# Kernel tuning notes

Measured on AMD Instinct MI355X. Metric: run time of the kernel, lower is better.

Reference implementation:

```python
import jax, jax.numpy as jnp
import numpy as np

B, S, H = 8, 2048, 1024
NEG = 1.0e10


def setup_inputs() -> dict:
    key = jax.random.key(0)
    ks = jax.random.split(key, 9)
    scale = 1.0 / np.sqrt(H)
    x = jax.random.normal(ks[0], (B, S, H), dtype=jnp.float32)
    Wq = jax.random.normal(ks[1], (H, H), dtype=jnp.float32) * scale
    bq = jnp.zeros((H,), dtype=jnp.float32)
    Wk = jax.random.normal(ks[2], (H, H), dtype=jnp.float32) * scale
    bk = jnp.zeros((H,), dtype=jnp.float32)
    Wv = jax.random.normal(ks[3], (H, H), dtype=jnp.float32) * scale
    bv = jnp.zeros((H,), dtype=jnp.float32)
    gamma = jnp.ones((H,), dtype=jnp.float32)
    beta = jnp.zeros((H,), dtype=jnp.float32)
    return {"x": x, "Wq": Wq, "bq": bq, "Wk": Wk, "bk": bk,
            "Wv": Wv, "bv": bv, "gamma": gamma, "beta": beta}


def _layernorm(y, gamma, beta, eps=1e-5):
    mu = jnp.mean(y, axis=-1, keepdims=True)
    var = jnp.var(y, axis=-1, keepdims=True)
    return (y - mu) * jax.lax.rsqrt(var + eps) * gamma + beta


def reference(x, Wq, bq, Wk, bk, Wv, bv, gamma, beta):
    # QKV projections (single head, no 1/sqrt(d) scaling, per original code)
    q = x @ Wq + bq                       # [B, S, H]
    k = x @ Wk + bk                       # [B, S, H]
    v = x @ Wv + bv                       # [B, S, H]
    scores = jnp.einsum('bsh,bth->bst', q, k)   # [B, S, S]
    # non-standard multiplicative-subtractive causal mask
    mask = jnp.tril(jnp.ones((S, S), dtype=scores.dtype))  # [S, S]
    scores = scores * mask - NEG * (1.0 - mask)
    probs = jax.nn.softmax(scores, axis=-1)
    attn = jnp.einsum('bst,bth->bsh', probs, v)
    return _layernorm(v + attn, gamma, beta)
```

## Files before the change

### kernel.cpp

```cpp
#include <hip/hip_runtime.h>

#define SQ 2048
#define HD 1024
#define NB 8
#define NTOT (NB*SQ)
#define NT2 8
#define NTRI2 36
#define CE ((long long)NTRI2*65536)

typedef _Float16 f16x8 __attribute__((ext_vector_type(8)));
typedef float f32x4 __attribute__((ext_vector_type(4)));
typedef short s16x8 __attribute__((ext_vector_type(8)));
typedef unsigned short u16;

__device__ __forceinline__ u16 f2h(float x){
  _Float16 h = (_Float16)x;
  u16 u; __builtin_memcpy(&u, &h, 2); return u;
}

#define STG(gp, lp) __builtin_amdgcn_global_load_lds( \
    (const __attribute__((address_space(1))) unsigned*)(gp), \
    (__attribute__((address_space(3))) unsigned*)(lp), 16, 0, 0)

template<int EPI>
__global__ __launch_bounds__(512, 2)
void gemm8(const u16* __restrict__ A, const u16* __restrict__ B,
           float* Cf, u16* Ch, u16* Vt,
           const float* __restrict__ b0, const float* __restrict__ b1,
           const float* __restrict__ b2,
           int K, int lda, int ldb, int ldc,
           long long sA, long long sB, long long sC)
{
  const int z = blockIdx.z;
  int bi, bj, tri = 0;
  if (EPI == 1){
    int t = blockIdx.x;
    int i = (int)((sqrtf(8.f * (float)t + 1.f) - 1.f) * 0.5f);
    while ((i + 1) * (i + 2) / 2 <= t) ++i;
    while (i * (i + 1) / 2 > t) --i;
    bi = i;  bj = t - i * (i + 1) / 2;  tri = t;
  } else {
    bi = blockIdx.x;  bj = blockIdx.y;
    if (EPI == 2) tri = bi * (bi + 1) / 2;
  }

  __shared__ short lds[65536];

  const int tid  = threadIdx.x;
  const int lane = tid & 63, w = tid >> 6;
  const int wm2 = w >> 2, wn4 = w & 3;
  const int lrow = lane & 15, kgrp = lane >> 4;

  const long long rowA = (long long)bi * 256;
  const long long colB = (long long)bj * 256;

  const int rt = tid >> 3;
  const int gs = (tid & 7) ^ (rt & 7);

  const u16 *sAp[4], *sBp[4];
  if (EPI == 2){
    const u16* Pb = A + (long long)z * sA + (long long)tri * 65536;
    #pragma unroll
    for (int i = 0; i < 4; i++)
      sAp[i] = Pb + (i * 64 + rt) * 256 + gs * 8;
  } else {
    const u16* Ab = A + (EPI == 0 ? 0LL : (long long)z * sA);
    #pragma unroll
    for (int i = 0; i < 4; i++)
      sAp[i] = Ab + (rowA + i * 64 + rt) * (long long)lda + gs * 8;
  }
  {
    const u16* Bb = B + (long long)z * sB;
    #pragma unroll
    for (int i = 0; i < 4; i++)
      sBp[i] = Bb + (colB + i * 64 + rt) * (long long)ldb + gs * 8;
  }

  #define ADST(buf,i) (lds + (buf) * 32768 +         (i) * 4096 + w * 512)
  #define BDST(buf,i) (lds + (buf) * 32768 + 16384 + (i) * 4096 + w * 512)

  const int fl = lrow & 7;
  const int swzk[2] = { ((0 + kgrp) ^ fl) * 8, ((4 + kgrp) ^ fl) * 8 };
  const int arow = (wm2 * 128 + lrow) * 64;
  const int brow = 16384 + (wn4 * 64 + lrow) * 64;

  f32x4 acc[8][4];
  const f32x4 zf = {0.f, 0.f, 0.f, 0.f};
  #pragma unroll
  for (int m = 0; m < 8; m++)
    #pragma unroll
    for (int n = 0; n < 4; n++) acc[m][n] = zf;

  int KT = K >> 6;
  if (EPI == 2){ int t = (bi + 1) * 4; if (t < KT) KT = t; }

  auto advance = [&](int tS){
    long long advA = 64;
    if (EPI == 2) advA = ((tS & 3) == 3) ? (65536 - 192) : 64;
    #pragma unroll
    for (int i = 0; i < 4; i++){ sAp[i] += advA; sBp[i] += 64; }
  };

  #pragma unroll
  for (int i = 0; i < 4; i++) STG(sAp[i], ADST(0, i));
  #pragma unroll
  for (int i = 0; i < 4; i++) STG(sBp[i], BDST(0, i));
  advance(0);
  __syncthreads();

  int cur = 0;
  for (int kt = 0; kt < KT; ++kt){
    const bool pf = (kt + 1 < KT);
    const short* Ab = lds + cur * 32768;
    const int nb = cur ^ 1;

    #pragma unroll
    for (int qm = 0; qm < 2; qm++){
      f16x8 aq[4][2];
      #pragma unroll
      for (int m4 = 0; m4 < 4; m4++)
        #pragma unroll
        for (int ks = 0; ks < 2; ks++)
          aq[m4][ks] = *(const f16x8*)(Ab + arow + (qm * 4 + m4) * 1024 + swzk[ks]);

      #pragma unroll
      for (int qn = 0; qn < 2; qn++){
        if (pf && qm == 0 && qn == 0){
          #pragma unroll
          for (int i = 0; i < 4; i++) STG(sAp[i], ADST(nb, i));
        }
        if (pf && qm == 0 && qn == 1){
          #pragma unroll
          for (int i = 0; i < 4; i++) STG(sBp[i], BDST(nb, i));
        }
        f16x8 bq[2][2];
        #pragma unroll
        for (int n2 = 0; n2 < 2; n2++)
          #pragma unroll
          for (int ks = 0; ks < 2; ks++)
            bq[n2][ks] = *(const f16x8*)(Ab + brow + (qn * 2 + n2) * 1024 + swzk[ks]);

        __builtin_amdgcn_s_setprio(1);
        #pragma unroll
        for (int n2 = 0; n2 < 2; n2++)
          #pragma unroll
          for (int m4 = 0; m4 < 4; m4++)
            #pragma unroll
            for (int ks = 0; ks < 2; ks++)
              acc[qm * 4 + m4][qn * 2 + n2] =
                __builtin_amdgcn_mfma_f32_16x16x32_f16(aq[m4][ks], bq[n2][ks],
                                                       acc[qm * 4 + m4][qn * 2 + n2], 0, 0, 0);
        __builtin_amdgcn_s_setprio(0);
        __builtin_amdgcn_s_barrier();
      }
    }
    if (pf) advance(kt + 1);
    __syncthreads();
    cur ^= 1;
  }
  #undef ADST
  #undef BDST

  if (EPI == 0){
    if (z < 2){
      u16* c = Ch + (long long)z * sC;
      const float* bias = z ? b1 : b0;
      #pragma unroll
      for (int n = 0; n < 4; n++){
        int col = (int)colB + wn4 * 64 + n * 16 + lrow;
        float ba = bias[col];
        #pragma unroll
        for (int m = 0; m < 8; m++){
          long long r = rowA + wm2 * 128 + m * 16 + kgrp * 4;
          #pragma unroll
          for (int j = 0; j < 4; j++)
            c[(r + j) * ldc + col] = f2h(acc[m][n][j] + ba);
        }
      }
    } else {
      #pragma unroll
      for (int n = 0; n < 4; n++){
        int col = (int)colB + wn4 * 64 + n * 16 + lrow;
        float ba = b2[col];
        #pragma unroll
        for (int m = 0; m < 8; m++){
          long long r = rowA + wm2 * 128 + m * 16 + kgrp * 4;
          int bb = (int)(r >> 11);
          int s  = (int)(r & 2047);
          u16* vtc = Vt + ((long long)bb * HD + col) * SQ + s;
          #pragma unroll
          for (int j = 0; j < 4; j++){
            float v = acc[m][n][j] + ba;
            Cf[(r + j) * ldc + col] = v;
            vtc[j] = f2h(v);
          }
        }
      }
    }
  } else if (EPI == 1){
    float* cf = Cf + (long long)z * sC + (long long)tri * 65536;
    #pragma unroll
    for (int n = 0; n < 4; n++){
      int col = wn4 * 64 + n * 16 + lrow;
      #pragma unroll
      for (int m = 0; m < 8; m++){
        int r = wm2 * 128 + m * 16 + kgrp * 4;
        #pragma unroll
        for (int j = 0; j < 4; j++)
          cf[(r + j) * 256 + col] = acc[m][n][j];
      }
    }
  } else {
    float* cf = Cf + (long long)z * sC;
    #pragma unroll
    for (int n = 0; n < 4; n++){
      int col = (int)colB + wn4 * 64 + n * 16 + lrow;
      #pragma unroll
      for (int m = 0; m < 8; m++){
        long long r = rowA + wm2 * 128 + m * 16 + kgrp * 4;
        #pragma unroll
        for (int j = 0; j < 4; j++){
          long long o = (r + j) * ldc + col;
          cf[o] = acc[m][n][j] + cf[o];
        }
      }
    }
  }
}

__global__ __launch_bounds__(256)
void prep_x(const float* __restrict__ X, u16* __restrict__ Xh)
{
  const long long n8 = (long long)NTOT * HD / 8;
  for (long long i = (long long)blockIdx.x * 256 + threadIdx.x; i < n8;
       i += (long long)gridDim.x * 256){
    const float* p = X + i * 8;
    float4 a = *(const float4*)p;
    float4 b = *(const float4*)(p + 4);
    float f[8] = {a.x, a.y, a.z, a.w, b.x, b.y, b.z, b.w};
    s16x8 h;
    #pragma unroll
    for (int j = 0; j < 8; j++) h[j] = (short)f2h(f[j]);
    *(s16x8*)&Xh[i * 8] = h;
  }
}

__global__ void prep_w(const float* __restrict__ Wq, const float* __restrict__ Wk,
                       const float* __restrict__ Wv, u16* __restrict__ Wt)
{
  __shared__ float t[32][33];
  const float* Win = (blockIdx.z == 0) ? Wq : (blockIdx.z == 1) ? Wk : Wv;
  const size_t zo = (size_t)blockIdx.z * HD * HD;
  int n0 = blockIdx.x * 32, k0 = blockIdx.y * 32;
  int tx = threadIdx.x, ty = threadIdx.y;
  #pragma unroll
  for (int i = 0; i < 4; i++)
    t[ty + 8*i][tx] = Win[(size_t)(k0 + ty + 8*i) * HD + n0 + tx];
  __syncthreads();
  #pragma unroll
  for (int i = 0; i < 4; i++)
    Wt[zo + (size_t)(n0 + ty + 8*i) * HD + k0 + tx] = f2h(t[tx][ty + 8*i]);
}

__global__ __launch_bounds__(256)
void softmax_causal(const float* __restrict__ SC, u16* __restrict__ P)
{
  const int s = blockIdx.x;
  const int i = s >> 8;
  const int tri = i * (i + 1) / 2;
  const long long base = (long long)blockIdx.y * CE + (long long)tri * 65536
                       + (long long)(s & 255) * 256;
  const float* scb = SC + base;
  u16* pb = P + base;

  __shared__ float buf[SQ];
  __shared__ float red[4];
  const int tid = threadIdx.x, lane = tid & 63, wid = tid >> 6;

  float m = -3.4e38f;
  for (int t = tid; t <= s; t += 256){
    float v = scb[(t >> 8) * 65536 + (t & 255)];
    buf[t] = v; m = fmaxf(m, v);
  }
  #pragma unroll
  for (int o = 32; o; o >>= 1) m = fmaxf(m, __shfl_xor(m, o));
  if (lane == 0) red[wid] = m;
  __syncthreads();
  m = fmaxf(fmaxf(red[0], red[1]), fmaxf(red[2], red[3]));
  __syncthreads();

  float sum = 0.f;
  for (int t = tid; t <= s; t += 256){ float e = __expf(buf[t] - m); buf[t] = e; sum += e; }
  #pragma unroll
  for (int o = 32; o; o >>= 1) sum += __shfl_xor(sum, o);
  if (lane == 0) red[wid] = sum;
  __syncthreads();
  sum = red[0] + red[1] + red[2] + red[3];
  const float inv = 1.f / sum;

  const int lim = (i + 1) << 8;
  for (int t = tid; t < lim; t += 256)
    pb[(t >> 8) * 65536 + (t & 255)] = (t <= s) ? f2h(buf[t] * inv) : (u16)0;
}

__global__ __launch_bounds__(256)
void layernorm_inplace(float* __restrict__ Y, const float* __restrict__ gamma,
                       const float* __restrict__ beta)
{
  float* y = Y + (long long)blockIdx.x * HD;
  const int tid = threadIdx.x, lane = tid & 63, wid = tid >> 6;
  float xv[4];
  float s = 0.f, ss = 0.f;
  #pragma unroll
  for (int i = 0; i < 4; i++){
    float v = y[tid + i * 256];
    xv[i] = v; s += v; ss += v * v;
  }
  #pragma unroll
  for (int o = 32; o; o >>= 1){ s += __shfl_xor(s, o); ss += __shfl_xor(ss, o); }
  __shared__ float r1[4], r2[4];
  if (lane == 0){ r1[wid] = s; r2[wid] = ss; }
  __syncthreads();
  s  = r1[0] + r1[1] + r1[2] + r1[3];
  ss = r2[0] + r2[1] + r2[2] + r2[3];
  const float mu   = s * (1.f / HD);
  const float var  = ss * (1.f / HD) - mu * mu;
  const float rstd = rsqrtf(var + 1e-5f);
  #pragma unroll
  for (int i = 0; i < 4; i++){
    int c = tid + i * 256;
    y[c] = (xv[i] - mu) * rstd * gamma[c] + beta[c];
  }
}

extern "C" void kernel_launch(void* const* d_in, const int* in_sizes, int n_in,
                              void* d_out, int out_size, void* d_ws, size_t ws_size,
                              hipStream_t stream)
{
  const float* x     = (const float*)d_in[0];
  const float* Wq    = (const float*)d_in[1];
  const float* bq    = (const float*)d_in[2];
  const float* Wk    = (const float*)d_in[3];
  const float* bk    = (const float*)d_in[4];
  const float* Wv    = (const float*)d_in[5];
  const float* bv    = (const float*)d_in[6];
  const float* gamma = (const float*)d_in[7];
  const float* beta  = (const float*)d_in[8];
  float* out = (float*)d_out;

  char* wsp = (char*)d_ws;
  size_t off = 0;
  auto alloc = [&](size_t bytes) -> char* {
    char* p = wsp + off;
    off = (off + bytes + 255) & ~(size_t)255;
    return p;
  };

  u16* Wt = (u16*)alloc(3ULL * HD * HD * 2);
  u16* QK = (u16*)alloc(2ULL * NTOT * HD * 2);
  u16* Vt = (u16*)alloc((size_t)NB * HD * SQ * 2);

  size_t rem = (ws_size > off) ? (ws_size - off) : 0;
  size_t perb = (size_t)CE * 6;
  int G = (int)(rem / perb);
  if (G > NB) G = NB;
  if (G < 1)  G = 1;
  u16*   xh = (u16*)(wsp + off);
  float* SC = (float*)(wsp + off);
  u16*   P  = (u16*)(wsp + off + (size_t)G * CE * 4);

  u16* Qh = QK;
  u16* Kh = QK + (size_t)NTOT * HD;
  float* V = out;

  prep_x<<<dim3(2048), dim3(256), 0, stream>>>(x, xh);
  prep_w<<<dim3(HD/32, HD/32, 3), dim3(32, 8), 0, stream>>>(Wq, Wk, Wv, Wt);

  gemm8<0><<<dim3(NTOT/256, HD/256, 3), 512, 0, stream>>>(
      xh, Wt, V, QK, Vt, bq, bk, bv,
      HD, HD, HD, HD,
      0LL, (long long)HD * HD, (long long)NTOT * HD);

  for (int g0 = 0; g0 < NB; g0 += G){
    int g = (G < NB - g0) ? G : (NB - g0);
    gemm8<1><<<dim3(NTRI2, 1, g), 512, 0, stream>>>(
        Qh + (size_t)g0 * SQ * HD, Kh + (size_t)g0 * SQ * HD,
        SC, nullptr, nullptr, nullptr, nullptr, nullptr,
        HD, HD, HD, 256,
        (long long)SQ * HD, (long long)SQ * HD, CE);
    softmax_causal<<<dim3(SQ, g), 256, 0, stream>>>(SC, P);
    gemm8<2><<<dim3(NT2, HD/256, g), 512, 0, stream>>>(
        P, Vt + (size_t)g0 * HD * SQ,
        out + (size_t)g0 * SQ * HD, nullptr, nullptr, nullptr, nullptr, nullptr,
        SQ, 256, SQ, HD,
        CE, (long long)HD * SQ, (long long)SQ * HD);
  }

  layernorm_inplace<<<dim3(NTOT), 256, 0, stream>>>(out, gamma, beta);
}
```

Measured before the change: 379.6 us.

## Switch GEMM mainloop to 4-stage K=32 pipeline with vmcnt-based waits

Replaces the double-buffered K=64 LDS pipeline with a four-stage ring of K=32 tiles, prefetching three stages ahead and waiting with explicit s_waitcnt vmcnt counts instead of full __syncthreads. The LDS layout and swizzle are reorganised so each wave reads its A/B fragments for a single K=32 step. The aim is to hide global-load latency better and cut barrier stalls, at the cost of more loop iterations, more barriers per unit of K, and reliance on exact vmcnt accounting for correctness.

```diff
diff --git a/kernel.cpp b/kernel.cpp
--- a/kernel.cpp
+++ b/kernel.cpp
@@ -44,7 +44,7 @@
     if (EPI == 2) tri = bi * (bi + 1) / 2;
   }
 
-  __shared__ short lds[65536];
+  __shared__ short lds[4 * 16384];
 
   const int tid  = threadIdx.x;
   const int lane = tid & 63, w = tid >> 6;
@@ -55,34 +55,32 @@
   const long long colB = (long long)bj * 256;
 
   const int rt = tid >> 3;
-  const int gs = (tid & 7) ^ (rt & 7);
-
-  const u16 *sAp[4], *sBp[4];
+  const int qp = (tid & 7) ^ (rt & 7);
+  const int kq = qp & 3;
+  const int rh = (qp >> 2) << 7;
+
+  const u16 *sAp[2], *sBp[2];
   if (EPI == 2){
     const u16* Pb = A + (long long)z * sA + (long long)tri * 65536;
     #pragma unroll
-    for (int i = 0; i < 4; i++)
-      sAp[i] = Pb + (i * 64 + rt) * 256 + gs * 8;
+    for (int i = 0; i < 2; i++)
+      sAp[i] = Pb + (i * 64 + rt + rh) * 256 + kq * 8;
   } else {
     const u16* Ab = A + (EPI == 0 ? 0LL : (long long)z * sA);
     #pragma unroll
-    for (int i = 0; i < 4; i++)
-      sAp[i] = Ab + (rowA + i * 64 + rt) * (long long)lda + gs * 8;
+    for (int i = 0; i < 2; i++)
+      sAp[i] = Ab + (rowA + i * 64 + rt + rh) * (long long)lda + kq * 8;
   }
   {
     const u16* Bb = B + (long long)z * sB;
     #pragma unroll
-    for (int i = 0; i < 4; i++)
-      sBp[i] = Bb + (colB + i * 64 + rt) * (long long)ldb + gs * 8;
-  }
-
-  #define ADST(buf,i) (lds + (buf) * 32768 +         (i) * 4096 + w * 512)
-  #define BDST(buf,i) (lds + (buf) * 32768 + 16384 + (i) * 4096 + w * 512)
-
-  const int fl = lrow & 7;
-  const int swzk[2] = { ((0 + kgrp) ^ fl) * 8, ((4 + kgrp) ^ fl) * 8 };
-  const int arow = (wm2 * 128 + lrow) * 64;
-  const int brow = 16384 + (wn4 * 64 + lrow) * 64;
+    for (int i = 0; i < 2; i++)
+      sBp[i] = Bb + (colB + i * 64 + rt + rh) * (long long)ldb + kq * 8;
+  }
+
+  const int aoff = lrow * 64 + ((((wm2 << 2) | kgrp) ^ (lrow & 7)) << 3);
+  const int boff = 8192 + ((wn4 & 1) * 64 + lrow) * 64
+                 + (((((wn4 >> 1) << 2) | kgrp) ^ (lrow & 7)) << 3);
 
   f32x4 acc[8][4];
   const f32x4 zf = {0.f, 0.f, 0.f, 0.f};
@@ -91,75 +89,68 @@
     #pragma unroll
     for (int n = 0; n < 4; n++) acc[m][n] = zf;
 
-  int KT = K >> 6;
-  if (EPI == 2){ int t = (bi + 1) * 4; if (t < KT) KT = t; }
-
+  int KT = K >> 5;
+  if (EPI == 2){ int t = (bi + 1) * 8; if (t < KT) KT = t; }
+
+  auto stage = [&](int b){
+    #pragma unroll
+    for (int i = 0; i < 2; i++) STG(sAp[i], lds + b * 16384 +        (i * 8 + w) * 512);
+    #pragma unroll
+    for (int i = 0; i < 2; i++) STG(sBp[i], lds + b * 16384 + 8192 + (i * 8 + w) * 512);
+  };
   auto advance = [&](int tS){
-    long long advA = 64;
-    if (EPI == 2) advA = ((tS & 3) == 3) ? (65536 - 192) : 64;
-    #pragma unroll
-    for (int i = 0; i < 4; i++){ sAp[i] += advA; sBp[i] += 64; }
+    long long advA = 32;
+    if (EPI == 2) advA = ((tS & 7) == 7) ? (65536 - 224) : 32;
+    sAp[0] += advA; sAp[1] += advA; sBp[0] += 32; sBp[1] += 32;
   };
 
-  #pragma unroll
-  for (int i = 0; i < 4; i++) STG(sAp[i], ADST(0, i));
-  #pragma unroll
-  for (int i = 0; i < 4; i++) STG(sBp[i], BDST(0, i));
-  advance(0);
-  __syncthreads();
-
-  int cur = 0;
+  stage(0); advance(0);
+  if (KT > 1){ stage(1); advance(1); }
+  if (KT > 2){ stage(2); advance(2); }
+  if (KT > 2)      { asm volatile("s_waitcnt vmcnt(8)" ::: "memory"); }
+  else if (KT > 1) { asm volatile("s_waitcnt vmcnt(4)" ::: "memory"); }
+  else             { asm volatile("s_waitcnt vmcnt(0)" ::: "memory"); }
+  __builtin_amdgcn_s_barrier();
+
   for (int kt = 0; kt < KT; ++kt){
-    const bool pf = (kt + 1 < KT);
-    const short* Ab = lds + cur * 32768;
-    const int nb = cur ^ 1;
-
-    #pragma unroll
-    for (int qm = 0; qm < 2; qm++){
-      f16x8 aq[4][2];
-      #pragma unroll
-      for (int m4 = 0; m4 < 4; m4++)
-        #pragma unroll
-        for (int ks = 0; ks < 2; ks++)
-          aq[m4][ks] = *(const f16x8*)(Ab + arow + (qm * 4 + m4) * 1024 + swzk[ks]);
-
-      #pragma unroll
-      for (int qn = 0; qn < 2; qn++){
-        if (pf && qm == 0 && qn == 0){
-          #pragma unroll
-          for (int i = 0; i < 4; i++) STG(sAp[i], ADST(nb, i));
-        }
-        if (pf && qm == 0 && qn == 1){
-          #pragma unroll
-          for (int i = 0; i < 4; i++) STG(sBp[i], BDST(nb, i));
-        }
-        f16x8 bq[2][2];
-        #pragma unroll
-        for (int n2 = 0; n2 < 2; n2++)
-          #pragma unroll
-          for (int ks = 0; ks < 2; ks++)
-            bq[n2][ks] = *(const f16x8*)(Ab + brow + (qn * 2 + n2) * 1024 + swzk[ks]);
-
-        __builtin_amdgcn_s_setprio(1);
-        #pragma unroll
-        for (int n2 = 0; n2 < 2; n2++)
-          #pragma unroll
-          for (int m4 = 0; m4 < 4; m4++)
-            #pragma unroll
-            for (int ks = 0; ks < 2; ks++)
-              acc[qm * 4 + m4][qn * 2 + n2] =
-                __builtin_amdgcn_mfma_f32_16x16x32_f16(aq[m4][ks], bq[n2][ks],
-                                                       acc[qm * 4 + m4][qn * 2 + n2], 0, 0, 0);
-        __builtin_amdgcn_s_setprio(0);
-        __builtin_amdgcn_s_barrier();
-      }
-    }
-    if (pf) advance(kt + 1);
-    __syncthreads();
-    cur ^= 1;
-  }
-  #undef ADST
-  #undef BDST
+    const short* Ab = lds + (kt & 3) * 16384;
+    if (kt + 3 < KT){ stage((kt + 3) & 3); advance(kt + 3); }
+
+    f16x8 bfr[4], af[4];
+    #pragma unroll
+    for (int n = 0; n < 4; n++)
+      bfr[n] = *(const f16x8*)(Ab + boff + n * 1024);
+    #pragma unroll
+    for (int m = 0; m < 4; m++)
+      af[m] = *(const f16x8*)(Ab + aoff + m * 1024);
+
+    __builtin_amdgcn_s_setprio(1);
+    #pragma unroll
+    for (int n = 0; n < 4; n++)
+      #pragma unroll
+      for (int m = 0; m < 4; m++)
+        acc[m][n] = __builtin_amdgcn_mfma_f32_16x16x32_f16(af[m], bfr[n], acc[m][n], 0, 0, 0);
+    __builtin_amdgcn_s_setprio(0);
+    __builtin_amdgcn_s_barrier();
+
+    #pragma unroll
+    for (int m = 0; m < 4; m++)
+      af[m] = *(const f16x8*)(Ab + aoff + (4 + m) * 1024);
+
+    __builtin_amdgcn_s_setprio(1);
+    #pragma unroll
+    for (int n = 0; n < 4; n++)
+      #pragma unroll
+      for (int m = 0; m < 4; m++)
+        acc[4 + m][n] = __builtin_amdgcn_mfma_f32_16x16x32_f16(af[m], bfr[n], acc[4 + m][n], 0, 0, 0);
+    __builtin_amdgcn_s_setprio(0);
+
+    const int rem = KT - 1 - kt;
+    if (rem >= 3)      { asm volatile("s_waitcnt vmcnt(8)" ::: "memory"); }
+    else if (rem == 2) { asm volatile("s_waitcnt vmcnt(4)" ::: "memory"); }
+    else if (rem == 1) { asm volatile("s_waitcnt vmcnt(0)" ::: "memory"); }
+    if (rem > 0) __builtin_amdgcn_s_barrier();
+  }
 
   if (EPI == 0){
     if (z < 2){
```

New measurement: 396.9 us. 4.6% more time.
